# Kernel optimization log

Measured on AMD Instinct MI355X. Metric: run time of the kernel, lower is better.

## Reference

```python
import jax, jax.numpy as jnp
import numpy as np

B, T, C_M, C_Z, H = 4, 1024, 256, 128, 8
DH = C_M // H  # dim_head = 32


def setup_inputs() -> dict:
    key = jax.random.key(0)
    ks = jax.random.split(key, 6)
    x = jax.random.normal(ks[0], (B, T, C_M), dtype=jnp.float32)
    bias_rep = jax.random.normal(ks[1], (T, T, C_Z), dtype=jnp.float32)
    s = 0.02
    Wqkv = jax.random.normal(ks[2], (C_M, 4 * H * DH), dtype=jnp.float32) * s
    W0 = jax.random.normal(ks[3], (H * DH, C_M), dtype=jnp.float32) * s
    Wb = jax.random.normal(ks[4], (C_Z, H), dtype=jnp.float32) * s
    bb = jax.random.normal(ks[5], (H,), dtype=jnp.float32) * s
    return {"x": x, "bias_rep": bias_rep, "Wqkv": Wqkv, "W0": W0, "Wb": Wb, "bb": bb}


def reference(x, bias_rep, Wqkv, W0, Wb, bb):
    b, t, _ = x.shape
    qkv = x @ Wqkv  # [b, t, 4*H*DH]
    # torch rearrange 'b t (d k h) -> k b h t d' with k=4, h=H: inner layout (d, k, h)
    qkv = qkv.reshape(b, t, DH, 4, H).transpose(3, 0, 4, 1, 2)  # [4, b, H, t, DH]
    q, k, v, g = qkv[0], qkv[1], qkv[2], qkv[3]
    scale = DH ** -0.5
    scores = jnp.einsum('bhid,bhjd->bhij', q, k) * scale  # [b, H, t, t]
    pair_bias = (bias_rep @ Wb + bb)  # [t, t, H]
    pair_bias = pair_bias.transpose(2, 0, 1)[None]  # [1, H, t, t]
    attn = jax.nn.softmax(scores + pair_bias, axis=-1)
    out = jnp.einsum('bhij,bhjd->bhid', attn, v)  # [b, H, t, DH]
    out = out * jax.nn.sigmoid(g)
    out = out.transpose(0, 2, 1, 3).reshape(b, t, H * DH)  # 'b h t d -> b t (h d)'
    return out @ W0
```

## Files before the change

kernel.cpp:

```cpp
#include <hip/hip_runtime.h>
#include <math.h>

#define T_SEQ 1024
#define CM 256
#define HEADS 8
#define DHH 32
#define NB 4
#define TT (T_SEQ * T_SEQ)

typedef __attribute__((ext_vector_type(8))) short bf16x8;
typedef __attribute__((ext_vector_type(4))) float f32x4;

__device__ __forceinline__ unsigned short f2bf(float f) {
    unsigned u = __builtin_bit_cast(unsigned, f);
    unsigned r = (u + 0x7FFFu + ((u >> 16) & 1u)) >> 16;
    return (unsigned short)r;
}

__device__ __forceinline__ bf16x8 cvt8(const float4 a0, const float4 a1) {
    bf16x8 t;
    t[0] = (short)f2bf(a0.x); t[1] = (short)f2bf(a0.y);
    t[2] = (short)f2bf(a0.z); t[3] = (short)f2bf(a0.w);
    t[4] = (short)f2bf(a1.x); t[5] = (short)f2bf(a1.y);
    t[6] = (short)f2bf(a1.z); t[7] = (short)f2bf(a1.w);
    return t;
}

__global__ __launch_bounds__(256) void transpose_cast_kernel(const float* __restrict__ W,
                                                             unsigned short* __restrict__ Wt,
                                                             int cols) {
    int o = blockIdx.x * 256 + threadIdx.x;
    int n = o >> 8, k = o & 255;
    Wt[o] = f2bf(W[k * cols + n]);
}

__global__ __launch_bounds__(256) void pad_wb_kernel(const float* __restrict__ Wb,
                                                     unsigned short* __restrict__ WbT) {
    int idx = blockIdx.x * 256 + threadIdx.x;
    int h = idx >> 7, k = idx & 127;
    WbT[idx] = (h < 8) ? f2bf(Wb[k * 8 + h]) : (unsigned short)0;
}

__global__ __launch_bounds__(256) void qkv_gemm_mfma(const float* __restrict__ x,
                                                     const unsigned short* __restrict__ Wt,
                                                     unsigned short* __restrict__ qb,
                                                     unsigned short* __restrict__ kb,
                                                     unsigned short* __restrict__ vT,
                                                     float* __restrict__ g) {
    const int tid = threadIdx.x;
    const int w = tid >> 6;
    const int lane = tid & 63;
    const int n16 = lane & 15;
    const int quad = lane >> 4;
    const int m0 = blockIdx.y * 64 + w * 16;
    const int h = blockIdx.x;
    const float scale = 0.17677669529663687f;

    bf16x8 afr[8];
    #pragma unroll
    for (int kc = 0; kc < 8; ++kc) {
        const float* src = &x[(m0 + n16) * 256 + kc * 32 + quad * 8];
        float4 a0 = *(const float4*)src;
        float4 a1 = *(const float4*)(src + 4);
        afr[kc] = cvt8(a0, a1);
    }

    #pragma unroll
    for (int s = 0; s < 8; ++s) {
        const int kk = s >> 1;
        const int dhi = s & 1;
        const int c = (dhi * 16 + n16) * 32 + kk * 8 + h;
        f32x4 acc = {0.f, 0.f, 0.f, 0.f};
        #pragma unroll
        for (int kc = 0; kc < 8; ++kc) {
            bf16x8 bfr = *(const bf16x8*)&Wt[c * 256 + kc * 32 + quad * 8];
            acc = __builtin_amdgcn_mfma_f32_16x16x32_bf16(afr[kc], bfr, acc, 0, 0, 0);
        }
        const int d = dhi * 16 + n16;
        #pragma unroll
        for (int r = 0; r < 4; ++r) {
            int m = m0 + quad * 4 + r;
            int b = m >> 10, t = m & 1023;
            int bh = b * HEADS + h;
            float val = acc[r];
            if (kk == 0)      qb[(bh * T_SEQ + t) * DHH + d] = f2bf(val * scale);
            else if (kk == 1) kb[(bh * T_SEQ + t) * DHH + d] = f2bf(val);
            else if (kk == 2) vT[(bh * DHH + d) * T_SEQ + t] = f2bf(val);
            else              g[(bh * T_SEQ + t) * DHH + d] = val;
        }
    }
}

__global__ __launch_bounds__(256) void pair_bias_mfma(const float* __restrict__ bias_rep,
                                                      const unsigned short* __restrict__ WbT,
                                                      const float* __restrict__ bb,
                                                      float* __restrict__ pb) {
    const int tid = threadIdx.x;
    const int w = tid >> 6;
    const int lane = tid & 63;
    const int n16 = lane & 15;
    const int quad = lane >> 4;
    const int p0 = blockIdx.x * 64 + w * 16;

    bf16x8 afr[4];
    #pragma unroll
    for (int kc = 0; kc < 4; ++kc) {
        const float* src = &bias_rep[(long long)(p0 + n16) * 128 + kc * 32 + quad * 8];
        float4 a0 = *(const float4*)src;
        float4 a1 = *(const float4*)(src + 4);
        afr[kc] = cvt8(a0, a1);
    }

    f32x4 acc = {0.f, 0.f, 0.f, 0.f};
    #pragma unroll
    for (int kc = 0; kc < 4; ++kc) {
        bf16x8 bfr = *(const bf16x8*)&WbT[n16 * 128 + kc * 32 + quad * 8];
        acc = __builtin_amdgcn_mfma_f32_16x16x32_bf16(afr[kc], bfr, acc, 0, 0, 0);
    }

    if (n16 < 8) {
        float bbv = bb[n16];
        #pragma unroll
        for (int r = 0; r < 4; ++r)
            pb[(long long)n16 * TT + p0 + quad * 4 + r] = acc[r] + bbv;
    }
}

__global__ __launch_bounds__(256) void attn_mfma(const unsigned short* __restrict__ qb,
                                                 const unsigned short* __restrict__ kb,
                                                 const unsigned short* __restrict__ vT,
                                                 const float* __restrict__ g,
                                                 const float* __restrict__ pb,
                                                 unsigned short* __restrict__ gated) {
    __shared__ unsigned short Ps[4][16][72];
    const int tid = threadIdx.x;
    const int w = tid >> 6;
    const int lane = tid & 63;
    const int n16 = lane & 15;
    const int quad = lane >> 4;
    const int it0 = blockIdx.x * 64;
    const int h = blockIdx.y, b = blockIdx.z;
    const int bh = b * HEADS + h;
    const int qrow0 = it0 + w * 16;

    bf16x8 qfr = *(const bf16x8*)&qb[(bh * T_SEQ + qrow0 + n16) * DHH + quad * 8];

    float m_i[4] = {-INFINITY, -INFINITY, -INFINITY, -INFINITY};
    float l_i[4] = {0.f, 0.f, 0.f, 0.f};
    f32x4 O0 = {0.f, 0.f, 0.f, 0.f};
    f32x4 O1 = {0.f, 0.f, 0.f, 0.f};

    for (int jt = 0; jt < 16; ++jt) {
        const int j0 = jt * 64;
        float pbv[4][4];
        #pragma unroll
        for (int s4 = 0; s4 < 4; ++s4)
            #pragma unroll
            for (int r = 0; r < 4; ++r)
                pbv[s4][r] = pb[h * TT + (qrow0 + quad * 4 + r) * T_SEQ + j0 + s4 * 16 + n16];

        f32x4 S[4];
        __builtin_amdgcn_s_setprio(1);
        #pragma unroll
        for (int s4 = 0; s4 < 4; ++s4) {
            bf16x8 kfr = *(const bf16x8*)&kb[(bh * T_SEQ + j0 + s4 * 16 + n16) * DHH + quad * 8];
            f32x4 z = {0.f, 0.f, 0.f, 0.f};
            S[s4] = __builtin_amdgcn_mfma_f32_16x16x32_bf16(qfr, kfr, z, 0, 0, 0);
        }
        __builtin_amdgcn_s_setprio(0);

        #pragma unroll
        for (int s4 = 0; s4 < 4; ++s4)
            #pragma unroll
            for (int r = 0; r < 4; ++r)
                S[s4][r] += pbv[s4][r];

        #pragma unroll
        for (int r = 0; r < 4; ++r) {
            float mx = fmaxf(fmaxf(S[0][r], S[1][r]), fmaxf(S[2][r], S[3][r]));
            mx = fmaxf(mx, __shfl_xor(mx, 1));
            mx = fmaxf(mx, __shfl_xor(mx, 2));
            mx = fmaxf(mx, __shfl_xor(mx, 4));
            mx = fmaxf(mx, __shfl_xor(mx, 8));
            float mnew = fmaxf(m_i[r], mx);
            float alpha = __expf(m_i[r] - mnew);
            m_i[r] = mnew;
            float lsum = 0.f;
            #pragma unroll
            for (int s4 = 0; s4 < 4; ++s4) {
                float p = __expf(S[s4][r] - mnew);
                S[s4][r] = p;
                lsum += p;
            }
            l_i[r] = l_i[r] * alpha + lsum;
            O0[r] *= alpha;
            O1[r] *= alpha;
        }

        #pragma unroll
        for (int s4 = 0; s4 < 4; ++s4)
            #pragma unroll
            for (int r = 0; r < 4; ++r)
                Ps[w][quad * 4 + r][s4 * 16 + n16] = f2bf(S[s4][r]);
        __builtin_amdgcn_s_setprio(1);
        #pragma unroll
        for (int kc = 0; kc < 2; ++kc) {
            bf16x8 pfr = *(const bf16x8*)&Ps[w][n16][kc * 32 + quad * 8];
            bf16x8 v0 = *(const bf16x8*)&vT[(bh * DHH + n16) * T_SEQ + j0 + kc * 32 + quad * 8];
            bf16x8 v1 = *(const bf16x8*)&vT[(bh * DHH + 16 + n16) * T_SEQ + j0 + kc * 32 + quad * 8];
            O0 = __builtin_amdgcn_mfma_f32_16x16x32_bf16(pfr, v0, O0, 0, 0, 0);
            O1 = __builtin_amdgcn_mfma_f32_16x16x32_bf16(pfr, v1, O1, 0, 0, 0);
        }
        __builtin_amdgcn_s_setprio(0);
    }

    #pragma unroll
    for (int r = 0; r < 4; ++r) {
        float lr = l_i[r];
        lr += __shfl_xor(lr, 1);
        lr += __shfl_xor(lr, 2);
        lr += __shfl_xor(lr, 4);
        lr += __shfl_xor(lr, 8);
        int t = qrow0 + quad * 4 + r;
        float linv = 1.f / lr;
        float g0 = g[(bh * T_SEQ + t) * DHH + n16];
        float g1 = g[(bh * T_SEQ + t) * DHH + 16 + n16];
        float o0 = O0[r] * linv / (1.f + __expf(-g0));
        float o1 = O1[r] * linv / (1.f + __expf(-g1));
        gated[(b * T_SEQ + t) * CM + h * DHH + n16] = f2bf(o0);
        gated[(b * T_SEQ + t) * CM + h * DHH + 16 + n16] = f2bf(o1);
    }
}

__global__ __launch_bounds__(64) void out_gemm_mfma(const unsigned short* __restrict__ gb,
                                                    const unsigned short* __restrict__ W0t,
                                                    float* __restrict__ y) {
    const int lane = threadIdx.x;
    const int n16 = lane & 15;
    const int quad = lane >> 4;
    const int m0 = blockIdx.x * 16;

    bf16x8 afr[8];
    #pragma unroll
    for (int kc = 0; kc < 8; ++kc)
        afr[kc] = *(const bf16x8*)&gb[(m0 + n16) * 256 + kc * 32 + quad * 8];

    #pragma unroll
    for (int s = 0; s < 16; ++s) {
        f32x4 acc = {0.f, 0.f, 0.f, 0.f};
        #pragma unroll
        for (int kc = 0; kc < 8; ++kc) {
            bf16x8 bfr = *(const bf16x8*)&W0t[(s * 16 + n16) * 256 + kc * 32 + quad * 8];
            acc = __builtin_amdgcn_mfma_f32_16x16x32_bf16(afr[kc], bfr, acc, 0, 0, 0);
        }
        #pragma unroll
        for (int r = 0; r < 4; ++r)
            y[(m0 + quad * 4 + r) * 256 + s * 16 + n16] = acc[r];
    }
}

extern "C" void kernel_launch(void* const* d_in, const int* in_sizes, int n_in,
                              void* d_out, int out_size, void* d_ws, size_t ws_size,
                              hipStream_t stream) {
    const float* x        = (const float*)d_in[0];
    const float* bias_rep = (const float*)d_in[1];
    const float* Wqkv     = (const float*)d_in[2];
    const float* W0       = (const float*)d_in[3];
    const float* Wb       = (const float*)d_in[4];
    const float* bb       = (const float*)d_in[5];

    char* ws = (char*)d_ws;
    float*          pb    = (float*)ws;                 ws += 8LL * 1024 * 1024 * 4;
    float*          g     = (float*)ws;                 ws += 4LL * 1024 * 1024;
    unsigned short* qb    = (unsigned short*)ws;        ws += 2LL * 1024 * 1024;
    unsigned short* kb    = (unsigned short*)ws;        ws += 2LL * 1024 * 1024;
    unsigned short* vT    = (unsigned short*)ws;        ws += 2LL * 1024 * 1024;
    unsigned short* gated = (unsigned short*)ws;        ws += 2LL * 1024 * 1024;
    unsigned short* Wt    = (unsigned short*)ws;        ws += 512LL * 1024;
    unsigned short* W0t   = (unsigned short*)ws;        ws += 128LL * 1024;
    unsigned short* WbT   = (unsigned short*)ws;
    float* y = (float*)d_out;

    transpose_cast_kernel<<<1024, 256, 0, stream>>>(Wqkv, Wt, 1024);
    transpose_cast_kernel<<<256, 256, 0, stream>>>(W0, W0t, 256);
    pad_wb_kernel<<<8, 256, 0, stream>>>(Wb, WbT);
    qkv_gemm_mfma<<<dim3(8, 64), 256, 0, stream>>>(x, Wt, qb, kb, vT, g);
    pair_bias_mfma<<<16384, 256, 0, stream>>>(bias_rep, WbT, bb, pb);
    attn_mfma<<<dim3(16, HEADS, NB), 256, 0, stream>>>(qb, kb, vT, g, pb, gated);
    out_gemm_mfma<<<256, 64, 0, stream>>>(gated, W0t, y);
}
```

Measured before the change: 804.3 us.

## Double-buffer attention loads, tile weight transposes, rebalance QKV and output GEMM grids

The attention loop now prefetches the next tile's pair-bias values and K fragments into alternating register buffers while the current tile computes, to hide global load latency. Weight transpose-cast uses an LDS-tiled kernel with coalesced float4 reads and ushort4 writes. The QKV GEMM processes two heads per block, halving the grid and reusing loaded x fragments. The output GEMM grid is split four ways over columns for more parallelism, at the cost of reloading A fragments four times. The double buffering raises register pressure, which may reduce occupancy.

```diff
diff --git a/kernel.cpp b/kernel.cpp
--- a/kernel.cpp
+++ b/kernel.cpp
@@ -26,12 +26,23 @@
     return t;
 }
 
-__global__ __launch_bounds__(256) void transpose_cast_kernel(const float* __restrict__ W,
-                                                             unsigned short* __restrict__ Wt,
-                                                             int cols) {
-    int o = blockIdx.x * 256 + threadIdx.x;
-    int n = o >> 8, k = o & 255;
-    Wt[o] = f2bf(W[k * cols + n]);
+__global__ __launch_bounds__(256) void transpose_cast_lds(const float* __restrict__ W,
+                                                          unsigned short* __restrict__ Wt,
+                                                          int cols) {
+    __shared__ float tile[32][33];
+    const int n0 = blockIdx.x * 32, k0 = blockIdx.y * 32;
+    const int r = threadIdx.x >> 3;
+    const int c4 = (threadIdx.x & 7) * 4;
+    float4 v = *(const float4*)&W[(k0 + r) * cols + n0 + c4];
+    tile[r][c4 + 0] = v.x; tile[r][c4 + 1] = v.y;
+    tile[r][c4 + 2] = v.z; tile[r][c4 + 3] = v.w;
+    __syncthreads();
+    ushort4 o;
+    o.x = f2bf(tile[c4 + 0][r]);
+    o.y = f2bf(tile[c4 + 1][r]);
+    o.z = f2bf(tile[c4 + 2][r]);
+    o.w = f2bf(tile[c4 + 3][r]);
+    *(ushort4*)&Wt[(n0 + r) * 256 + k0 + c4] = o;
 }
 
 __global__ __launch_bounds__(256) void pad_wb_kernel(const float* __restrict__ Wb,
@@ -53,7 +64,7 @@
     const int n16 = lane & 15;
     const int quad = lane >> 4;
     const int m0 = blockIdx.y * 64 + w * 16;
-    const int h = blockIdx.x;
+    const int hbase = blockIdx.x * 2;
     const float scale = 0.17677669529663687f;
 
     bf16x8 afr[8];
@@ -66,8 +77,9 @@
     }
 
     #pragma unroll
-    for (int s = 0; s < 8; ++s) {
-        const int kk = s >> 1;
+    for (int s = 0; s < 16; ++s) {
+        const int h = hbase + (s >> 3);
+        const int kk = (s >> 1) & 3;
         const int dhi = s & 1;
         const int c = (dhi * 16 + n16) * 32 + kk * 8 + h;
         f32x4 acc = {0.f, 0.f, 0.f, 0.f};
@@ -150,69 +162,83 @@
     f32x4 O0 = {0.f, 0.f, 0.f, 0.f};
     f32x4 O1 = {0.f, 0.f, 0.f, 0.f};
 
-    for (int jt = 0; jt < 16; ++jt) {
-        const int j0 = jt * 64;
-        float pbv[4][4];
-        #pragma unroll
-        for (int s4 = 0; s4 < 4; ++s4)
-            #pragma unroll
-            for (int r = 0; r < 4; ++r)
-                pbv[s4][r] = pb[h * TT + (qrow0 + quad * 4 + r) * T_SEQ + j0 + s4 * 16 + n16];
-
-        f32x4 S[4];
-        __builtin_amdgcn_s_setprio(1);
-        #pragma unroll
-        for (int s4 = 0; s4 < 4; ++s4) {
-            bf16x8 kfr = *(const bf16x8*)&kb[(bh * T_SEQ + j0 + s4 * 16 + n16) * DHH + quad * 8];
-            f32x4 z = {0.f, 0.f, 0.f, 0.f};
-            S[s4] = __builtin_amdgcn_mfma_f32_16x16x32_bf16(qfr, kfr, z, 0, 0, 0);
-        }
-        __builtin_amdgcn_s_setprio(0);
-
-        #pragma unroll
-        for (int s4 = 0; s4 < 4; ++s4)
-            #pragma unroll
-            for (int r = 0; r < 4; ++r)
-                S[s4][r] += pbv[s4][r];
-
-        #pragma unroll
-        for (int r = 0; r < 4; ++r) {
-            float mx = fmaxf(fmaxf(S[0][r], S[1][r]), fmaxf(S[2][r], S[3][r]));
-            mx = fmaxf(mx, __shfl_xor(mx, 1));
-            mx = fmaxf(mx, __shfl_xor(mx, 2));
-            mx = fmaxf(mx, __shfl_xor(mx, 4));
-            mx = fmaxf(mx, __shfl_xor(mx, 8));
-            float mnew = fmaxf(m_i[r], mx);
-            float alpha = __expf(m_i[r] - mnew);
-            m_i[r] = mnew;
-            float lsum = 0.f;
-            #pragma unroll
-            for (int s4 = 0; s4 < 4; ++s4) {
-                float p = __expf(S[s4][r] - mnew);
-                S[s4][r] = p;
-                lsum += p;
-            }
-            l_i[r] = l_i[r] * alpha + lsum;
-            O0[r] *= alpha;
-            O1[r] *= alpha;
-        }
-
-        #pragma unroll
-        for (int s4 = 0; s4 < 4; ++s4)
-            #pragma unroll
-            for (int r = 0; r < 4; ++r)
-                Ps[w][quad * 4 + r][s4 * 16 + n16] = f2bf(S[s4][r]);
-        __builtin_amdgcn_s_setprio(1);
-        #pragma unroll
-        for (int kc = 0; kc < 2; ++kc) {
-            bf16x8 pfr = *(const bf16x8*)&Ps[w][n16][kc * 32 + quad * 8];
-            bf16x8 v0 = *(const bf16x8*)&vT[(bh * DHH + n16) * T_SEQ + j0 + kc * 32 + quad * 8];
-            bf16x8 v1 = *(const bf16x8*)&vT[(bh * DHH + 16 + n16) * T_SEQ + j0 + kc * 32 + quad * 8];
-            O0 = __builtin_amdgcn_mfma_f32_16x16x32_bf16(pfr, v0, O0, 0, 0, 0);
-            O1 = __builtin_amdgcn_mfma_f32_16x16x32_bf16(pfr, v1, O1, 0, 0, 0);
-        }
-        __builtin_amdgcn_s_setprio(0);
-    }
+    float pbvA[4][4], pbvB[4][4];
+    bf16x8 kfrA[4], kfrB[4];
+
+#define PREFETCH(pbvX, kfrX, jtn) do {                                           \
+    const int jn_ = (jtn) & 15;                                                  \
+    const int jj_ = jn_ * 64;                                                    \
+    _Pragma("unroll")                                                            \
+    for (int s4 = 0; s4 < 4; ++s4) {                                             \
+        _Pragma("unroll")                                                        \
+        for (int r = 0; r < 4; ++r)                                              \
+            pbvX[s4][r] = pb[h * TT + (qrow0 + quad * 4 + r) * T_SEQ + jj_ + s4 * 16 + n16]; \
+        kfrX[s4] = *(const bf16x8*)&kb[(bh * T_SEQ + jj_ + s4 * 16 + n16) * DHH + quad * 8]; \
+    }                                                                            \
+} while (0)
+
+#define TILE_BODY(pbvC, kfrC, jtc) do {                                          \
+    const int j0_ = (jtc) * 64;                                                  \
+    f32x4 S[4];                                                                  \
+    __builtin_amdgcn_s_setprio(1);                                               \
+    _Pragma("unroll")                                                            \
+    for (int s4 = 0; s4 < 4; ++s4) {                                             \
+        f32x4 z = {0.f, 0.f, 0.f, 0.f};                                          \
+        S[s4] = __builtin_amdgcn_mfma_f32_16x16x32_bf16(qfr, kfrC[s4], z, 0, 0, 0); \
+    }                                                                            \
+    __builtin_amdgcn_s_setprio(0);                                               \
+    _Pragma("unroll")                                                            \
+    for (int s4 = 0; s4 < 4; ++s4)                                               \
+        _Pragma("unroll")                                                        \
+        for (int r = 0; r < 4; ++r)                                              \
+            S[s4][r] += pbvC[s4][r];                                             \
+    _Pragma("unroll")                                                            \
+    for (int r = 0; r < 4; ++r) {                                                \
+        float mx = fmaxf(fmaxf(S[0][r], S[1][r]), fmaxf(S[2][r], S[3][r]));      \
+        mx = fmaxf(mx, __shfl_xor(mx, 1));                                       \
+        mx = fmaxf(mx, __shfl_xor(mx, 2));                                       \
+        mx = fmaxf(mx, __shfl_xor(mx, 4));                                       \
+        mx = fmaxf(mx, __shfl_xor(mx, 8));                                       \
+        float mnew = fmaxf(m_i[r], mx);                                          \
+        float alpha = __expf(m_i[r] - mnew);                                     \
+        m_i[r] = mnew;                                                           \
+        float lsum = 0.f;                                                        \
+        _Pragma("unroll")                                                        \
+        for (int s4 = 0; s4 < 4; ++s4) {                                         \
+            float p = __expf(S[s4][r] - mnew);                                   \
+            S[s4][r] = p;                                                        \
+            lsum += p;                                                           \
+        }                                                                        \
+        l_i[r] = l_i[r] * alpha + lsum;                                          \
+        O0[r] *= alpha;                                                          \
+        O1[r] *= alpha;                                                          \
+    }                                                                            \
+    _Pragma("unroll")                                                            \
+    for (int s4 = 0; s4 < 4; ++s4)                                               \
+        _Pragma("unroll")                                                        \
+        for (int r = 0; r < 4; ++r)                                              \
+            Ps[w][quad * 4 + r][s4 * 16 + n16] = f2bf(S[s4][r]);                 \
+    __builtin_amdgcn_s_setprio(1);                                               \
+    _Pragma("unroll")                                                            \
+    for (int kc = 0; kc < 2; ++kc) {                                             \
+        bf16x8 pfr = *(const bf16x8*)&Ps[w][n16][kc * 32 + quad * 8];            \
+        bf16x8 v0 = *(const bf16x8*)&vT[(bh * DHH + n16) * T_SEQ + j0_ + kc * 32 + quad * 8]; \
+        bf16x8 v1 = *(const bf16x8*)&vT[(bh * DHH + 16 + n16) * T_SEQ + j0_ + kc * 32 + quad * 8]; \
+        O0 = __builtin_amdgcn_mfma_f32_16x16x32_bf16(pfr, v0, O0, 0, 0, 0);      \
+        O1 = __builtin_amdgcn_mfma_f32_16x16x32_bf16(pfr, v1, O1, 0, 0, 0);      \
+    }                                                                            \
+    __builtin_amdgcn_s_setprio(0);                                               \
+} while (0)
+
+    PREFETCH(pbvA, kfrA, 0);
+    for (int jj = 0; jj < 16; jj += 2) {
+        PREFETCH(pbvB, kfrB, jj + 1);
+        TILE_BODY(pbvA, kfrA, jj);
+        PREFETCH(pbvA, kfrA, jj + 2);
+        TILE_BODY(pbvB, kfrB, jj + 1);
+    }
+#undef PREFETCH
+#undef TILE_BODY
 
     #pragma unroll
     for (int r = 0; r < 4; ++r) {
@@ -238,7 +264,8 @@
     const int lane = threadIdx.x;
     const int n16 = lane & 15;
     const int quad = lane >> 4;
-    const int m0 = blockIdx.x * 16;
+    const int m0 = (blockIdx.x >> 2) * 16;
+    const int sb = (blockIdx.x & 3) * 4;
 
     bf16x8 afr[8];
     #pragma unroll
@@ -246,7 +273,8 @@
         afr[kc] = *(const bf16x8*)&gb[(m0 + n16) * 256 + kc * 32 + quad * 8];
 
     #pragma unroll
-    for (int s = 0; s < 16; ++s) {
+    for (int si = 0; si < 4; ++si) {
+        const int s = sb + si;
         f32x4 acc = {0.f, 0.f, 0.f, 0.f};
         #pragma unroll
         for (int kc = 0; kc < 8; ++kc) {
@@ -281,11 +309,11 @@
     unsigned short* WbT   = (unsigned short*)ws;
     float* y = (float*)d_out;
 
-    transpose_cast_kernel<<<1024, 256, 0, stream>>>(Wqkv, Wt, 1024);
-    transpose_cast_kernel<<<256, 256, 0, stream>>>(W0, W0t, 256);
+    transpose_cast_lds<<<dim3(32, 8), 256, 0, stream>>>(Wqkv, Wt, 1024);
+    transpose_cast_lds<<<dim3(8, 8), 256, 0, stream>>>(W0, W0t, 256);
     pad_wb_kernel<<<8, 256, 0, stream>>>(Wb, WbT);
-    qkv_gemm_mfma<<<dim3(8, 64), 256, 0, stream>>>(x, Wt, qb, kb, vT, g);
+    qkv_gemm_mfma<<<dim3(4, 64), 256, 0, stream>>>(x, Wt, qb, kb, vT, g);
     pair_bias_mfma<<<16384, 256, 0, stream>>>(bias_rep, WbT, bb, pb);
     attn_mfma<<<dim3(16, HEADS, NB), 256, 0, stream>>>(qb, kb, vT, g, pb, gated);
-    out_gemm_mfma<<<256, 64, 0, stream>>>(gated, W0t, y);
-}
+    out_gemm_mfma<<<1024, 64, 0, stream>>>(gated, W0t, y);
+}
```

Result: faster. 757.4 us (-5.8%).
